# Kernel tuning notes

Measured on AMD Instinct MI355X. Metric: run time of the kernel, lower is better.

## Reference

```python
import jax, jax.numpy as jnp
import numpy as np

ROUTING_ITERS = 3
EPS = 1e-9


def squash(s, axis=-1):
    sq_norm = jnp.sum(s * s, axis=axis, keepdims=True)
    scale = sq_norm / (1.0 + sq_norm)
    return scale * s / jnp.sqrt(sq_norm + EPS)


def setup_inputs() -> dict:
    key = jax.random.key(0)
    k_u, k_w = jax.random.split(key)
    B, P, C, OUT, IN = 256, 2048, 10, 16, 8
    u = jax.random.normal(k_u, (B, P, IN), dtype=jnp.float32)
    W = 0.01 * jax.random.normal(k_w, (1, P, C, OUT, IN), dtype=jnp.float32)
    return {"u": u, "W": W}


def reference(u, W):
    # u: [B, P, IN], W: [1, P, C, OUT, IN]
    # u_hat[b,p,c,o] = sum_i W[0,p,c,o,i] * u[b,p,i]
    u_hat = jnp.einsum('pcoi,bpi->bpco', W[0], u)  # [B, P, C, OUT]
    B, P, C, _ = u_hat.shape
    b = jnp.zeros((B, P, C), dtype=u_hat.dtype)
    v = None
    for _ in range(ROUTING_ITERS):
        c = jax.nn.softmax(b, axis=2)                     # [B, P, C]
        s = jnp.einsum('bpc,bpco->bco', c, u_hat)         # [B, C, OUT]
        v = squash(s, axis=-1)                            # [B, C, OUT]
        b = b + jnp.einsum('bpco,bco->bpc', u_hat, v)     # agreement update
    return v
```

## Files before the change

kernel.cpp:

```cpp
#include <hip/hip_runtime.h>
#include <hip/hip_fp16.h>


#define Bn 256
#define Pn 2048
#define Cn 10
#define On 16
#define In 8
#define ROW 160
#define BT 64
#define PPB 16
#define NPT (Pn / PPB)
#define TPB 512
#define GRID ((Bn / BT) * NPT)

typedef _Float16 f16x8 __attribute__((ext_vector_type(8)));
typedef _Float16 h2f __attribute__((ext_vector_type(2)));
typedef float f32x4 __attribute__((ext_vector_type(4)));

__device__ __forceinline__ void gl_lds16(const void* g, void* l) {
  __builtin_amdgcn_global_load_lds(
      (const __attribute__((address_space(1))) unsigned int*)g,
      (__attribute__((address_space(3))) unsigned int*)l, 16, 0, 0);
}

__device__ __forceinline__ h2f pack2(float a, float b) {
  __half2 t = __floats2half2_rn(a, b);
  return *reinterpret_cast<h2f*>(&t);
}

__global__ __launch_bounds__(256) void k_prepw(const float* __restrict__ W,
                                               _Float16* __restrict__ Wh) {
  const size_t base = (size_t)blockIdx.x * 1280;
#pragma unroll
  for (int r = 0; r < 5; ++r) {
    const int i = threadIdx.x + 256 * r;
    Wh[base + i] = (_Float16)W[base + i];
  }
}

__global__ __launch_bounds__(256) void k_prepu(const float* __restrict__ u,
                                               _Float16* __restrict__ uT) {
  const int p2 = blockIdx.x * 2;
  const int b = threadIdx.x;
  const float4* src = reinterpret_cast<const float4*>(u + ((size_t)b * Pn + p2) * In);
  const float4 q0 = src[0], q1 = src[1], q2 = src[2], q3 = src[3];
  f16x8 o0, o1;
  o0[0] = (_Float16)q0.x; o0[1] = (_Float16)q0.y; o0[2] = (_Float16)q0.z; o0[3] = (_Float16)q0.w;
  o0[4] = (_Float16)q1.x; o0[5] = (_Float16)q1.y; o0[6] = (_Float16)q1.z; o0[7] = (_Float16)q1.w;
  o1[0] = (_Float16)q2.x; o1[1] = (_Float16)q2.y; o1[2] = (_Float16)q2.z; o1[3] = (_Float16)q2.w;
  o1[4] = (_Float16)q3.x; o1[5] = (_Float16)q3.y; o1[6] = (_Float16)q3.z; o1[7] = (_Float16)q3.w;
  *reinterpret_cast<f16x8*>(uT + ((size_t)p2 * Bn + b) * In) = o0;
  *reinterpret_cast<f16x8*>(uT + ((size_t)(p2 + 1) * Bn + b) * In) = o1;
}

template <int MODE>
__global__ __launch_bounds__(TPB, 2) void k_cap(const _Float16* __restrict__ uT,
                                                const _Float16* __restrict__ Wh,
                                                const float* __restrict__ s1,
                                                const float* __restrict__ s2,
                                                float* __restrict__ part) {
  __shared__ float arena[10368];
  _Float16* wH = reinterpret_cast<_Float16*>(arena);
  const int x = blockIdx.x;
  const int bt = x >> 7;
  const int pt = x & 127;
  const int tid = threadIdx.x;
  const int w = tid >> 6;
  const int pg = w >> 2;
  const int wq = w & 3;
  const int lane = tid & 63;
  const int col = lane & 15;
  const int quad = lane >> 4;
  const int b = bt * BT + wq * 16 + col;
  const int p0 = pt * PPB;

  {
    const char* src = reinterpret_cast<const char*>(Wh + (size_t)p0 * 1280);
    char* dst = reinterpret_cast<char*>(wH);
#pragma unroll
    for (int r = 0; r < 5; ++r)
      gl_lds16(src + r * 8192 + tid * 16, dst + r * 8192 + tid * 16);
  }

  h2f vh[Cn][2];
  if (MODE >= 1) {
    const float4* spA = reinterpret_cast<const float4*>(s1 + (size_t)b * ROW);
    const float4* spB = reinterpret_cast<const float4*>(s2 + (size_t)b * ROW);
#pragma unroll
    for (int c = 0; c < Cn; ++c) {
      const float4 a0 = spA[c * 4 + 0], a1 = spA[c * 4 + 1];
      const float4 a2 = spA[c * 4 + 2], a3 = spA[c * 4 + 3];
      float sqA = a0.x * a0.x + a0.y * a0.y + a0.z * a0.z + a0.w * a0.w;
      sqA += a1.x * a1.x + a1.y * a1.y + a1.z * a1.z + a1.w * a1.w;
      sqA += a2.x * a2.x + a2.y * a2.y + a2.z * a2.z + a2.w * a2.w;
      sqA += a3.x * a3.x + a3.y * a3.y + a3.z * a3.z + a3.w * a3.w;
      sqA *= 0.01f;
      const float facA = 0.1f * (sqA / (1.f + sqA)) / sqrtf(sqA + 1e-9f);
      const float4 qa = spA[c * 4 + quad];
      float v0 = facA * qa.x, v1_ = facA * qa.y;
      float v2_ = facA * qa.z, v3_ = facA * qa.w;
      if (MODE == 2) {
        const float4 b0 = spB[c * 4 + 0], b1 = spB[c * 4 + 1];
        const float4 b2 = spB[c * 4 + 2], b3 = spB[c * 4 + 3];
        float sqB = b0.x * b0.x + b0.y * b0.y + b0.z * b0.z + b0.w * b0.w;
        sqB += b1.x * b1.x + b1.y * b1.y + b1.z * b1.z + b1.w * b1.w;
        sqB += b2.x * b2.x + b2.y * b2.y + b2.z * b2.z + b2.w * b2.w;
        sqB += b3.x * b3.x + b3.y * b3.y + b3.z * b3.z + b3.w * b3.w;
        const float facB = (sqB / (1.f + sqB)) / sqrtf(sqB + 1e-9f);
        const float4 qb = spB[c * 4 + quad];
        v0 += facB * qb.x; v1_ += facB * qb.y;
        v2_ += facB * qb.z; v3_ += facB * qb.w;
      }
      vh[c][0] = pack2(v0, v1_);
      vh[c][1] = pack2(v2_, v3_);
    }
  }

  f32x4 acc[Cn];
  const f32x4 zc = {0.f, 0.f, 0.f, 0.f};
#pragma unroll
  for (int c = 0; c < Cn; ++c) acc[c] = zc;

  const _Float16* urow = uT + ((size_t)(p0 + pg * 8) * Bn + b) * In;
  f16x8 uf = *reinterpret_cast<const f16x8*>(urow);
  const f16x8 zb = {0, 0, 0, 0, 0, 0, 0, 0};
  const bool isq0 = (quad == 0);

  __syncthreads();

  for (int ip = 0; ip < 8; ++ip) {
    f16x8 ufn = uf;
    if (ip + 1 < 8)
      ufn = *reinterpret_cast<const f16x8*>(urow + (size_t)(ip + 1) * Bn * In);
    const f16x8 ub = isq0 ? uf : zb;
    const _Float16* wp = wH + (pg * 8 + ip) * 1280 + col * 8;

    if (MODE == 0) {
#pragma unroll
      for (int c = 0; c < Cn; ++c) {
        const f16x8 aW = *reinterpret_cast<const f16x8*>(wp + c * 128);
        acc[c] = __builtin_amdgcn_mfma_f32_16x16x32_f16(aW, ub, acc[c], 0, 0, 0);
      }
    } else {
      float lf[Cn];
      h2f uhh[Cn][2];
#pragma unroll
      for (int c = 0; c < Cn; ++c) {
        const f16x8 aW = *reinterpret_cast<const f16x8*>(wp + c * 128);
        const f32x4 uh =
            __builtin_amdgcn_mfma_f32_16x16x32_f16(aW, ub, zc, 0, 0, 0);
        float lp = uh[0] * (float)vh[c][0][0];
        lp = __builtin_fmaf(uh[1], (float)vh[c][0][1], lp);
        lp = __builtin_fmaf(uh[2], (float)vh[c][1][0], lp);
        lp = __builtin_fmaf(uh[3], (float)vh[c][1][1], lp);
        lf[c] = lp;
        uhh[c][0] = pack2(uh[0], uh[1]);
        uhh[c][1] = pack2(uh[2], uh[3]);
      }
#pragma unroll
      for (int c = 0; c < Cn; ++c) {
        lf[c] += __shfl_xor(lf[c], 16, 64);
        lf[c] += __shfl_xor(lf[c], 32, 64);
      }
      float m = fmaxf(fmaxf(__builtin_fmaf(0.f, 0.f, lf[0]), lf[1]), lf[2]);
      m = fmaxf(m, fmaxf(fmaxf(lf[3], lf[4]), fmaxf(lf[5], lf[6])));
      m = fmaxf(m, fmaxf(fmaxf(lf[7], lf[8]), lf[9]));
      float ss = 0.f;
#pragma unroll
      for (int c = 0; c < Cn; ++c) {
        lf[c] = __expf(lf[c] - m);
        ss += lf[c];
      }
      const float inv = 1.f / ss;
#pragma unroll
      for (int c = 0; c < Cn; ++c) {
        const float cv = lf[c] * inv;
        acc[c][0] = __builtin_fmaf(cv, (float)uhh[c][0][0], acc[c][0]);
        acc[c][1] = __builtin_fmaf(cv, (float)uhh[c][0][1], acc[c][1]);
        acc[c][2] = __builtin_fmaf(cv, (float)uhh[c][1][0], acc[c][2]);
        acc[c][3] = __builtin_fmaf(cv, (float)uhh[c][1][1], acc[c][3]);
      }
    }
    uf = ufn;
  }

  __syncthreads();
  float* sAcc = arena;
  const int row = wq * 16 + col;
  if (pg == 1) {
    float* dst = &sAcc[row * 162 + quad * 4];
#pragma unroll
    for (int c = 0; c < Cn; ++c)
      *reinterpret_cast<f32x4*>(dst + c * 16) = acc[c];
  }
  __syncthreads();
  if (pg == 0) {
    const float* srcp = &sAcc[row * 162 + quad * 4];
    float* pb = part + ((size_t)x * BT + row) * ROW;
#pragma unroll
    for (int c = 0; c < Cn; ++c) {
      f32x4 t = *reinterpret_cast<const f32x4*>(srcp + c * 16);
      t = t + acc[c];
      *reinterpret_cast<f32x4*>(pb + c * 16 + quad * 4) = t;
    }
  }
}

__global__ __launch_bounds__(256) void k_red(const float* __restrict__ part,
                                             float* __restrict__ s) {
  const int cell = blockIdx.x * 256 + threadIdx.x;
  const int chunk = blockIdx.y;
  const int b = cell / 160, rem = cell - 160 * b;
  const int bt = b >> 6, bl = b & 63;
  const float* p0 =
      part + ((size_t)(bt * NPT + chunk * 32) * BT + bl) * ROW + rem;
  float a0 = 0.f, a1 = 0.f, a2 = 0.f, a3 = 0.f;
  float a4 = 0.f, a5 = 0.f, a6 = 0.f, a7 = 0.f;
#pragma unroll
  for (int pt = 0; pt < 32; pt += 8) {
    a0 += p0[(size_t)(pt + 0) * BT * ROW];
    a1 += p0[(size_t)(pt + 1) * BT * ROW];
    a2 += p0[(size_t)(pt + 2) * BT * ROW];
    a3 += p0[(size_t)(pt + 3) * BT * ROW];
    a4 += p0[(size_t)(pt + 4) * BT * ROW];
    a5 += p0[(size_t)(pt + 5) * BT * ROW];
    a6 += p0[(size_t)(pt + 6) * BT * ROW];
    a7 += p0[(size_t)(pt + 7) * BT * ROW];
  }
  atomicAdd(&s[cell], ((a0 + a1) + (a2 + a3)) + ((a4 + a5) + (a6 + a7)));
}

__global__ __launch_bounds__(256) void k_out(const float* __restrict__ s,
                                             float* __restrict__ out) {
  const int gi = blockIdx.x * 256 + threadIdx.x;
  const int b = gi / 10, c = gi - 10 * b;
  const float* sp = s + (size_t)b * ROW + c * 16;
  float sq = 0.f;
#pragma unroll
  for (int o = 0; o < On; ++o) { const float xx = sp[o]; sq += xx * xx; }
  const float fac = (sq / (1.f + sq)) / sqrtf(sq + 1e-9f);
  float* op = out + (size_t)b * ROW + c * 16;
#pragma unroll
  for (int o = 0; o < On; ++o) op[o] = fac * sp[o];
}

extern "C" void kernel_launch(void* const* d_in, const int* in_sizes, int n_in,
                              void* d_out, int out_size, void* d_ws, size_t ws_size,
                              hipStream_t stream) {
  (void)in_sizes; (void)n_in; (void)out_size;
  const float* u = (const float*)d_in[0];
  const float* W = (const float*)d_in[1];
  float* out = (float*)d_out;
  float* s1 = (float*)d_ws;
  float* s2 = s1 + (size_t)Bn * ROW;
  float* s3 = s2 + (size_t)Bn * ROW;
  float* part = s3 + (size_t)Bn * ROW;
  _Float16* Wh = (_Float16*)(part + (size_t)GRID * BT * ROW);
  _Float16* uTp = Wh + (size_t)Pn * Cn * On * In;
  const size_t need =
      ((size_t)3 * Bn * ROW + (size_t)GRID * BT * ROW) * sizeof(float) +
      ((size_t)Pn * Cn * On * In + (size_t)Pn * Bn * In) * sizeof(_Float16);
  if (ws_size < need) return;
  hipMemsetAsync(s1, 0, (size_t)3 * Bn * ROW * sizeof(float), stream);
  k_prepw<<<Pn, 256, 0, stream>>>(W, Wh);
  k_prepu<<<Pn / 2, 256, 0, stream>>>(u, uTp);
  k_cap<0><<<GRID, TPB, 0, stream>>>(uTp, Wh, s1, s1, part);
  k_red<<<dim3(160, 4), 256, 0, stream>>>(part, s1);
  k_cap<1><<<GRID, TPB, 0, stream>>>(uTp, Wh, s1, s1, part);
  k_red<<<dim3(160, 4), 256, 0, stream>>>(part, s2);
  k_cap<2><<<GRID, TPB, 0, stream>>>(uTp, Wh, s1, s2, part);
  k_red<<<dim3(160, 4), 256, 0, stream>>>(part, s3);
  k_out<<<10, 256, 0, stream>>>(s3, out);
}
```

Measured before the change: 224.7 us.

## Halve k_cap block size, loop all 16 P per wave, drop LDS cross-group reduction

The capsule kernel now runs 256 threads (4 waves) per block instead of 512. Each wave processes all 16 P values, two at a time, rather than splitting them between two wave groups. This removes the shared-memory reduction and its two extra barriers at the end, and gives each wave two independent MFMA/softmax chains per iteration for more instruction-level parallelism. The costs are fewer waves per block, higher register pressure from doubled live state, and a longer serial loop per wave.

```diff
diff --git a/kernel.cpp b/kernel.cpp
--- a/kernel.cpp
+++ b/kernel.cpp
@@ -11,7 +11,7 @@
 #define BT 64
 #define PPB 16
 #define NPT (Pn / PPB)
-#define TPB 512
+#define TPB 256
 #define GRID ((Bn / BT) * NPT)
 
 typedef _Float16 f16x8 __attribute__((ext_vector_type(8)));
@@ -60,27 +60,24 @@
                                                 const float* __restrict__ s1,
                                                 const float* __restrict__ s2,
                                                 float* __restrict__ part) {
-  __shared__ float arena[10368];
-  _Float16* wH = reinterpret_cast<_Float16*>(arena);
+  __shared__ _Float16 wH[PPB * 1280];
   const int x = blockIdx.x;
   const int bt = x >> 7;
   const int pt = x & 127;
   const int tid = threadIdx.x;
   const int w = tid >> 6;
-  const int pg = w >> 2;
-  const int wq = w & 3;
   const int lane = tid & 63;
   const int col = lane & 15;
   const int quad = lane >> 4;
-  const int b = bt * BT + wq * 16 + col;
+  const int b = bt * BT + w * 16 + col;
   const int p0 = pt * PPB;
 
   {
     const char* src = reinterpret_cast<const char*>(Wh + (size_t)p0 * 1280);
     char* dst = reinterpret_cast<char*>(wH);
 #pragma unroll
-    for (int r = 0; r < 5; ++r)
-      gl_lds16(src + r * 8192 + tid * 16, dst + r * 8192 + tid * 16);
+    for (int r = 0; r < 10; ++r)
+      gl_lds16(src + r * 4096 + tid * 16, dst + r * 4096 + tid * 16);
   }
 
   h2f vh[Cn][2];
@@ -122,89 +119,104 @@
 #pragma unroll
   for (int c = 0; c < Cn; ++c) acc[c] = zc;
 
-  const _Float16* urow = uT + ((size_t)(p0 + pg * 8) * Bn + b) * In;
-  f16x8 uf = *reinterpret_cast<const f16x8*>(urow);
+  const _Float16* urow = uT + ((size_t)p0 * Bn + b) * In;
+  f16x8 ufA = *reinterpret_cast<const f16x8*>(urow);
+  f16x8 ufB = *reinterpret_cast<const f16x8*>(urow + (size_t)Bn * In);
   const f16x8 zb = {0, 0, 0, 0, 0, 0, 0, 0};
   const bool isq0 = (quad == 0);
 
   __syncthreads();
 
-  for (int ip = 0; ip < 8; ++ip) {
-    f16x8 ufn = uf;
-    if (ip + 1 < 8)
-      ufn = *reinterpret_cast<const f16x8*>(urow + (size_t)(ip + 1) * Bn * In);
-    const f16x8 ub = isq0 ? uf : zb;
-    const _Float16* wp = wH + (pg * 8 + ip) * 1280 + col * 8;
+  for (int ip = 0; ip < PPB; ip += 2) {
+    f16x8 nfA = ufA, nfB = ufB;
+    if (ip + 2 < PPB) {
+      nfA = *reinterpret_cast<const f16x8*>(urow + (size_t)(ip + 2) * Bn * In);
+      nfB = *reinterpret_cast<const f16x8*>(urow + (size_t)(ip + 3) * Bn * In);
+    }
+    const f16x8 ubA = isq0 ? ufA : zb;
+    const f16x8 ubB = isq0 ? ufB : zb;
+    const _Float16* wpA = wH + (size_t)ip * 1280 + col * 8;
+    const _Float16* wpB = wpA + 1280;
 
     if (MODE == 0) {
 #pragma unroll
       for (int c = 0; c < Cn; ++c) {
-        const f16x8 aW = *reinterpret_cast<const f16x8*>(wp + c * 128);
-        acc[c] = __builtin_amdgcn_mfma_f32_16x16x32_f16(aW, ub, acc[c], 0, 0, 0);
+        const f16x8 aWA = *reinterpret_cast<const f16x8*>(wpA + c * 128);
+        const f16x8 aWB = *reinterpret_cast<const f16x8*>(wpB + c * 128);
+        acc[c] = __builtin_amdgcn_mfma_f32_16x16x32_f16(aWA, ubA, acc[c], 0, 0, 0);
+        acc[c] = __builtin_amdgcn_mfma_f32_16x16x32_f16(aWB, ubB, acc[c], 0, 0, 0);
       }
     } else {
-      float lf[Cn];
-      h2f uhh[Cn][2];
-#pragma unroll
-      for (int c = 0; c < Cn; ++c) {
-        const f16x8 aW = *reinterpret_cast<const f16x8*>(wp + c * 128);
-        const f32x4 uh =
-            __builtin_amdgcn_mfma_f32_16x16x32_f16(aW, ub, zc, 0, 0, 0);
-        float lp = uh[0] * (float)vh[c][0][0];
-        lp = __builtin_fmaf(uh[1], (float)vh[c][0][1], lp);
-        lp = __builtin_fmaf(uh[2], (float)vh[c][1][0], lp);
-        lp = __builtin_fmaf(uh[3], (float)vh[c][1][1], lp);
-        lf[c] = lp;
-        uhh[c][0] = pack2(uh[0], uh[1]);
-        uhh[c][1] = pack2(uh[2], uh[3]);
-      }
-#pragma unroll
-      for (int c = 0; c < Cn; ++c) {
-        lf[c] += __shfl_xor(lf[c], 16, 64);
-        lf[c] += __shfl_xor(lf[c], 32, 64);
-      }
-      float m = fmaxf(fmaxf(__builtin_fmaf(0.f, 0.f, lf[0]), lf[1]), lf[2]);
-      m = fmaxf(m, fmaxf(fmaxf(lf[3], lf[4]), fmaxf(lf[5], lf[6])));
-      m = fmaxf(m, fmaxf(fmaxf(lf[7], lf[8]), lf[9]));
-      float ss = 0.f;
-#pragma unroll
-      for (int c = 0; c < Cn; ++c) {
-        lf[c] = __expf(lf[c] - m);
-        ss += lf[c];
-      }
-      const float inv = 1.f / ss;
-#pragma unroll
-      for (int c = 0; c < Cn; ++c) {
-        const float cv = lf[c] * inv;
-        acc[c][0] = __builtin_fmaf(cv, (float)uhh[c][0][0], acc[c][0]);
-        acc[c][1] = __builtin_fmaf(cv, (float)uhh[c][0][1], acc[c][1]);
-        acc[c][2] = __builtin_fmaf(cv, (float)uhh[c][1][0], acc[c][2]);
-        acc[c][3] = __builtin_fmaf(cv, (float)uhh[c][1][1], acc[c][3]);
+      float lfA[Cn], lfB[Cn];
+      h2f uhA[Cn][2], uhB[Cn][2];
+#pragma unroll
+      for (int c = 0; c < Cn; ++c) {
+        const f16x8 aWA = *reinterpret_cast<const f16x8*>(wpA + c * 128);
+        const f16x8 aWB = *reinterpret_cast<const f16x8*>(wpB + c * 128);
+        const f32x4 dA =
+            __builtin_amdgcn_mfma_f32_16x16x32_f16(aWA, ubA, zc, 0, 0, 0);
+        const f32x4 dB =
+            __builtin_amdgcn_mfma_f32_16x16x32_f16(aWB, ubB, zc, 0, 0, 0);
+        float la = dA[0] * (float)vh[c][0][0];
+        la = __builtin_fmaf(dA[1], (float)vh[c][0][1], la);
+        la = __builtin_fmaf(dA[2], (float)vh[c][1][0], la);
+        la = __builtin_fmaf(dA[3], (float)vh[c][1][1], la);
+        lfA[c] = la;
+        float lb = dB[0] * (float)vh[c][0][0];
+        lb = __builtin_fmaf(dB[1], (float)vh[c][0][1], lb);
+        lb = __builtin_fmaf(dB[2], (float)vh[c][1][0], lb);
+        lb = __builtin_fmaf(dB[3], (float)vh[c][1][1], lb);
+        lfB[c] = lb;
+        uhA[c][0] = pack2(dA[0], dA[1]);
+        uhA[c][1] = pack2(dA[2], dA[3]);
+        uhB[c][0] = pack2(dB[0], dB[1]);
+        uhB[c][1] = pack2(dB[2], dB[3]);
+      }
+#pragma unroll
+      for (int c = 0; c < Cn; ++c) {
+        lfA[c] += __shfl_xor(lfA[c], 16, 64);
+        lfB[c] += __shfl_xor(lfB[c], 16, 64);
+        lfA[c] += __shfl_xor(lfA[c], 32, 64);
+        lfB[c] += __shfl_xor(lfB[c], 32, 64);
+      }
+      float mA = fmaxf(fmaxf(lfA[0], lfA[1]), fmaxf(lfA[2], lfA[3]));
+      float mB = fmaxf(fmaxf(lfB[0], lfB[1]), fmaxf(lfB[2], lfB[3]));
+      mA = fmaxf(mA, fmaxf(fmaxf(lfA[4], lfA[5]), fmaxf(lfA[6], lfA[7])));
+      mB = fmaxf(mB, fmaxf(fmaxf(lfB[4], lfB[5]), fmaxf(lfB[6], lfB[7])));
+      mA = fmaxf(mA, fmaxf(lfA[8], lfA[9]));
+      mB = fmaxf(mB, fmaxf(lfB[8], lfB[9]));
+      float ssA = 0.f, ssB = 0.f;
+#pragma unroll
+      for (int c = 0; c < Cn; ++c) {
+        lfA[c] = __expf(lfA[c] - mA);
+        ssA += lfA[c];
+        lfB[c] = __expf(lfB[c] - mB);
+        ssB += lfB[c];
+      }
+      const float invA = 1.f / ssA;
+      const float invB = 1.f / ssB;
+#pragma unroll
+      for (int c = 0; c < Cn; ++c) {
+        const float cvA = lfA[c] * invA;
+        const float cvB = lfB[c] * invB;
+        float t0 = __builtin_fmaf(cvA, (float)uhA[c][0][0], acc[c][0]);
+        float t1 = __builtin_fmaf(cvA, (float)uhA[c][0][1], acc[c][1]);
+        float t2 = __builtin_fmaf(cvA, (float)uhA[c][1][0], acc[c][2]);
+        float t3 = __builtin_fmaf(cvA, (float)uhA[c][1][1], acc[c][3]);
+        acc[c][0] = __builtin_fmaf(cvB, (float)uhB[c][0][0], t0);
+        acc[c][1] = __builtin_fmaf(cvB, (float)uhB[c][0][1], t1);
+        acc[c][2] = __builtin_fmaf(cvB, (float)uhB[c][1][0], t2);
+        acc[c][3] = __builtin_fmaf(cvB, (float)uhB[c][1][1], t3);
       }
     }
-    uf = ufn;
-  }
-
-  __syncthreads();
-  float* sAcc = arena;
-  const int row = wq * 16 + col;
-  if (pg == 1) {
-    float* dst = &sAcc[row * 162 + quad * 4];
-#pragma unroll
-    for (int c = 0; c < Cn; ++c)
-      *reinterpret_cast<f32x4*>(dst + c * 16) = acc[c];
-  }
-  __syncthreads();
-  if (pg == 0) {
-    const float* srcp = &sAcc[row * 162 + quad * 4];
-    float* pb = part + ((size_t)x * BT + row) * ROW;
-#pragma unroll
-    for (int c = 0; c < Cn; ++c) {
-      f32x4 t = *reinterpret_cast<const f32x4*>(srcp + c * 16);
-      t = t + acc[c];
-      *reinterpret_cast<f32x4*>(pb + c * 16 + quad * 4) = t;
-    }
-  }
+    ufA = nfA;
+    ufB = nfB;
+  }
+
+  float* pb = part + ((size_t)x * BT + w * 16 + col) * ROW;
+#pragma unroll
+  for (int c = 0; c < Cn; ++c)
+    *reinterpret_cast<f32x4*>(pb + c * 16 + quad * 4) = acc[c];
 }
 
 __global__ __launch_bounds__(256) void k_red(const float* __restrict__ part,
```

Result: faster. 184.4 us (-17.9%).

## Restructure capsule routing to independent per-wave tiles with precomputed squashed v

Applied to the files above, without the earlier changes.

Drops the LDS staging of W and the cross-wave LDS reduction in the routing kernel. Each wave now handles its own 16-batch by 8-capsule tile, reads W straight from global memory, and writes its partial sums straight out, which doubles the partial buffer and the reduction chunks. A new small kernel computes the squashed v vectors once in fp16, so the main kernel no longer recomputes the squash norms in every block. The cost is more global and L2 traffic for W, because it is no longer shared across waves through LDS, and a larger reduction over partials.

```diff
diff --git a/kernel.cpp b/kernel.cpp
--- a/kernel.cpp
+++ b/kernel.cpp
@@ -8,21 +8,14 @@
 #define On 16
 #define In 8
 #define ROW 160
-#define BT 64
-#define PPB 16
-#define NPT (Pn / PPB)
-#define TPB 512
-#define GRID ((Bn / BT) * NPT)
+#define PPW 8
+#define NPT (Pn / PPW)
+#define TPB 256
+#define GRID (16 * NPT / 4)
 
 typedef _Float16 f16x8 __attribute__((ext_vector_type(8)));
 typedef _Float16 h2f __attribute__((ext_vector_type(2)));
 typedef float f32x4 __attribute__((ext_vector_type(4)));
-
-__device__ __forceinline__ void gl_lds16(const void* g, void* l) {
-  __builtin_amdgcn_global_load_lds(
-      (const __attribute__((address_space(1))) unsigned int*)g,
-      (__attribute__((address_space(3))) unsigned int*)l, 16, 0, 0);
-}
 
 __device__ __forceinline__ h2f pack2(float a, float b) {
   __half2 t = __floats2half2_rn(a, b);
@@ -54,66 +47,74 @@
   *reinterpret_cast<f16x8*>(uT + ((size_t)(p2 + 1) * Bn + b) * In) = o1;
 }
 
+template <int M>
+__global__ __launch_bounds__(256) void k_vprep(const float* __restrict__ sA,
+                                               const float* __restrict__ sB,
+                                               _Float16* __restrict__ vT) {
+  const int g = blockIdx.x * 256 + threadIdx.x;
+  const int b = g / 10, c = g - 10 * b;
+  const float4* pa = reinterpret_cast<const float4*>(sA + (size_t)b * ROW + c * 16);
+  const float4 a0 = pa[0], a1 = pa[1], a2 = pa[2], a3 = pa[3];
+  float sqA = a0.x * a0.x + a0.y * a0.y + a0.z * a0.z + a0.w * a0.w;
+  sqA += a1.x * a1.x + a1.y * a1.y + a1.z * a1.z + a1.w * a1.w;
+  sqA += a2.x * a2.x + a2.y * a2.y + a2.z * a2.z + a2.w * a2.w;
+  sqA += a3.x * a3.x + a3.y * a3.y + a3.z * a3.z + a3.w * a3.w;
+  sqA *= 0.01f;
+  const float facA = 0.1f * (sqA / (1.f + sqA)) / sqrtf(sqA + 1e-9f);
+  float v[16] = {facA * a0.x, facA * a0.y, facA * a0.z, facA * a0.w,
+                 facA * a1.x, facA * a1.y, facA * a1.z, facA * a1.w,
+                 facA * a2.x, facA * a2.y, facA * a2.z, facA * a2.w,
+                 facA * a3.x, facA * a3.y, facA * a3.z, facA * a3.w};
+  if (M == 2) {
+    const float4* pb = reinterpret_cast<const float4*>(sB + (size_t)b * ROW + c * 16);
+    const float4 b0 = pb[0], b1 = pb[1], b2 = pb[2], b3 = pb[3];
+    float sqB = b0.x * b0.x + b0.y * b0.y + b0.z * b0.z + b0.w * b0.w;
+    sqB += b1.x * b1.x + b1.y * b1.y + b1.z * b1.z + b1.w * b1.w;
+    sqB += b2.x * b2.x + b2.y * b2.y + b2.z * b2.z + b2.w * b2.w;
+    sqB += b3.x * b3.x + b3.y * b3.y + b3.z * b3.z + b3.w * b3.w;
+    const float facB = (sqB / (1.f + sqB)) / sqrtf(sqB + 1e-9f);
+    v[0] += facB * b0.x; v[1] += facB * b0.y; v[2] += facB * b0.z; v[3] += facB * b0.w;
+    v[4] += facB * b1.x; v[5] += facB * b1.y; v[6] += facB * b1.z; v[7] += facB * b1.w;
+    v[8] += facB * b2.x; v[9] += facB * b2.y; v[10] += facB * b2.z; v[11] += facB * b2.w;
+    v[12] += facB * b3.x; v[13] += facB * b3.y; v[14] += facB * b3.z; v[15] += facB * b3.w;
+  }
+#pragma unroll
+  for (int q = 0; q < 4; ++q) {
+    union { h2f h[2]; uint2 u2; } o;
+    o.h[0] = pack2(v[q * 4 + 0], v[q * 4 + 1]);
+    o.h[1] = pack2(v[q * 4 + 2], v[q * 4 + 3]);
+    *reinterpret_cast<uint2*>(vT + (size_t)((b * 4 + q) * 10 + c) * 4) = o.u2;
+  }
+}
+
 template <int MODE>
-__global__ __launch_bounds__(TPB, 2) void k_cap(const _Float16* __restrict__ uT,
-                                                const _Float16* __restrict__ Wh,
-                                                const float* __restrict__ s1,
-                                                const float* __restrict__ s2,
-                                                float* __restrict__ part) {
-  __shared__ float arena[10368];
-  _Float16* wH = reinterpret_cast<_Float16*>(arena);
+__global__ __launch_bounds__(TPB) void k_cap(const _Float16* __restrict__ uT,
+                                             const _Float16* __restrict__ Wh,
+                                             const _Float16* __restrict__ vT,
+                                             float* __restrict__ part) {
   const int x = blockIdx.x;
-  const int bt = x >> 7;
-  const int pt = x & 127;
   const int tid = threadIdx.x;
   const int w = tid >> 6;
-  const int pg = w >> 2;
-  const int wq = w & 3;
   const int lane = tid & 63;
+  const int gw = x * 4 + w;
+  const int btile = gw >> 8;
+  const int ptile = gw & 255;
   const int col = lane & 15;
   const int quad = lane >> 4;
-  const int b = bt * BT + wq * 16 + col;
-  const int p0 = pt * PPB;
-
-  {
-    const char* src = reinterpret_cast<const char*>(Wh + (size_t)p0 * 1280);
-    char* dst = reinterpret_cast<char*>(wH);
-#pragma unroll
-    for (int r = 0; r < 5; ++r)
-      gl_lds16(src + r * 8192 + tid * 16, dst + r * 8192 + tid * 16);
-  }
+  const int b = btile * 16 + col;
+  const int p0 = ptile * PPW;
 
   h2f vh[Cn][2];
   if (MODE >= 1) {
-    const float4* spA = reinterpret_cast<const float4*>(s1 + (size_t)b * ROW);
-    const float4* spB = reinterpret_cast<const float4*>(s2 + (size_t)b * ROW);
+    const f16x8* vsrc =
+        reinterpret_cast<const f16x8*>(vT + (size_t)(b * 4 + quad) * 40);
+    union { f16x8 v8[5]; h2f h[20]; } vu;
+#pragma unroll
+    for (int r = 0; r < 5; ++r) vu.v8[r] = vsrc[r];
 #pragma unroll
     for (int c = 0; c < Cn; ++c) {
-      const float4 a0 = spA[c * 4 + 0], a1 = spA[c * 4 + 1];
-      const float4 a2 = spA[c * 4 + 2], a3 = spA[c * 4 + 3];
-      float sqA = a0.x * a0.x + a0.y * a0.y + a0.z * a0.z + a0.w * a0.w;
-      sqA += a1.x * a1.x + a1.y * a1.y + a1.z * a1.z + a1.w * a1.w;
-      sqA += a2.x * a2.x + a2.y * a2.y + a2.z * a2.z + a2.w * a2.w;
-      sqA += a3.x * a3.x + a3.y * a3.y + a3.z * a3.z + a3.w * a3.w;
-      sqA *= 0.01f;
-      const float facA = 0.1f * (sqA / (1.f + sqA)) / sqrtf(sqA + 1e-9f);
-      const float4 qa = spA[c * 4 + quad];
-      float v0 = facA * qa.x, v1_ = facA * qa.y;
-      float v2_ = facA * qa.z, v3_ = facA * qa.w;
-      if (MODE == 2) {
-        const float4 b0 = spB[c * 4 + 0], b1 = spB[c * 4 + 1];
-        const float4 b2 = spB[c * 4 + 2], b3 = spB[c * 4 + 3];
-        float sqB = b0.x * b0.x + b0.y * b0.y + b0.z * b0.z + b0.w * b0.w;
-        sqB += b1.x * b1.x + b1.y * b1.y + b1.z * b1.z + b1.w * b1.w;
-        sqB += b2.x * b2.x + b2.y * b2.y + b2.z * b2.z + b2.w * b2.w;
-        sqB += b3.x * b3.x + b3.y * b3.y + b3.z * b3.z + b3.w * b3.w;
-        const float facB = (sqB / (1.f + sqB)) / sqrtf(sqB + 1e-9f);
-        const float4 qb = spB[c * 4 + quad];
-        v0 += facB * qb.x; v1_ += facB * qb.y;
-        v2_ += facB * qb.z; v3_ += facB * qb.w;
-      }
-      vh[c][0] = pack2(v0, v1_);
-      vh[c][1] = pack2(v2_, v3_);
+      vh[c][0] = vu.h[2 * c];
+      vh[c][1] = vu.h[2 * c + 1];
     }
   }
 
@@ -122,19 +123,16 @@
 #pragma unroll
   for (int c = 0; c < Cn; ++c) acc[c] = zc;
 
-  const _Float16* urow = uT + ((size_t)(p0 + pg * 8) * Bn + b) * In;
-  f16x8 uf = *reinterpret_cast<const f16x8*>(urow);
   const f16x8 zb = {0, 0, 0, 0, 0, 0, 0, 0};
   const bool isq0 = (quad == 0);
 
-  __syncthreads();
-
-  for (int ip = 0; ip < 8; ++ip) {
-    f16x8 ufn = uf;
-    if (ip + 1 < 8)
-      ufn = *reinterpret_cast<const f16x8*>(urow + (size_t)(ip + 1) * Bn * In);
+#pragma unroll 2
+  for (int ip = 0; ip < PPW; ++ip) {
+    const int p = p0 + ip;
+    const _Float16* wp = Wh + (size_t)p * 1280 + col * 8;
+    const f16x8 uf =
+        *reinterpret_cast<const f16x8*>(uT + ((size_t)p * Bn + b) * In);
     const f16x8 ub = isq0 ? uf : zb;
-    const _Float16* wp = wH + (pg * 8 + ip) * 1280 + col * 8;
 
     if (MODE == 0) {
 #pragma unroll
@@ -148,24 +146,24 @@
 #pragma unroll
       for (int c = 0; c < Cn; ++c) {
         const f16x8 aW = *reinterpret_cast<const f16x8*>(wp + c * 128);
-        const f32x4 uh =
+        const f32x4 d =
             __builtin_amdgcn_mfma_f32_16x16x32_f16(aW, ub, zc, 0, 0, 0);
-        float lp = uh[0] * (float)vh[c][0][0];
-        lp = __builtin_fmaf(uh[1], (float)vh[c][0][1], lp);
-        lp = __builtin_fmaf(uh[2], (float)vh[c][1][0], lp);
-        lp = __builtin_fmaf(uh[3], (float)vh[c][1][1], lp);
+        float lp = d[0] * (float)vh[c][0][0];
+        lp = __builtin_fmaf(d[1], (float)vh[c][0][1], lp);
+        lp = __builtin_fmaf(d[2], (float)vh[c][1][0], lp);
+        lp = __builtin_fmaf(d[3], (float)vh[c][1][1], lp);
         lf[c] = lp;
-        uhh[c][0] = pack2(uh[0], uh[1]);
-        uhh[c][1] = pack2(uh[2], uh[3]);
+        uhh[c][0] = pack2(d[0], d[1]);
+        uhh[c][1] = pack2(d[2], d[3]);
       }
 #pragma unroll
       for (int c = 0; c < Cn; ++c) {
         lf[c] += __shfl_xor(lf[c], 16, 64);
         lf[c] += __shfl_xor(lf[c], 32, 64);
       }
-      float m = fmaxf(fmaxf(__builtin_fmaf(0.f, 0.f, lf[0]), lf[1]), lf[2]);
-      m = fmaxf(m, fmaxf(fmaxf(lf[3], lf[4]), fmaxf(lf[5], lf[6])));
-      m = fmaxf(m, fmaxf(fmaxf(lf[7], lf[8]), lf[9]));
+      float m = fmaxf(fmaxf(lf[0], lf[1]), fmaxf(lf[2], lf[3]));
+      m = fmaxf(m, fmaxf(fmaxf(lf[4], lf[5]), fmaxf(lf[6], lf[7])));
+      m = fmaxf(m, fmaxf(lf[8], lf[9]));
       float ss = 0.f;
 #pragma unroll
       for (int c = 0; c < Cn; ++c) {
@@ -182,29 +180,12 @@
         acc[c][3] = __builtin_fmaf(cv, (float)uhh[c][1][1], acc[c][3]);
       }
     }
-    uf = ufn;
-  }
-
-  __syncthreads();
-  float* sAcc = arena;
-  const int row = wq * 16 + col;
-  if (pg == 1) {
-    float* dst = &sAcc[row * 162 + quad * 4];
-#pragma unroll
-    for (int c = 0; c < Cn; ++c)
-      *reinterpret_cast<f32x4*>(dst + c * 16) = acc[c];
-  }
-  __syncthreads();
-  if (pg == 0) {
-    const float* srcp = &sAcc[row * 162 + quad * 4];
-    float* pb = part + ((size_t)x * BT + row) * ROW;
-#pragma unroll
-    for (int c = 0; c < Cn; ++c) {
-      f32x4 t = *reinterpret_cast<const f32x4*>(srcp + c * 16);
-      t = t + acc[c];
-      *reinterpret_cast<f32x4*>(pb + c * 16 + quad * 4) = t;
-    }
-  }
+  }
+
+  float* pb = part + ((size_t)ptile * Bn + b) * ROW;
+#pragma unroll
+  for (int c = 0; c < Cn; ++c)
+    *reinterpret_cast<f32x4*>(pb + c * 16 + quad * 4) = acc[c];
 }
 
 __global__ __launch_bounds__(256) void k_red(const float* __restrict__ part,
@@ -212,21 +193,21 @@
   const int cell = blockIdx.x * 256 + threadIdx.x;
   const int chunk = blockIdx.y;
   const int b = cell / 160, rem = cell - 160 * b;
-  const int bt = b >> 6, bl = b & 63;
   const float* p0 =
-      part + ((size_t)(bt * NPT + chunk * 32) * BT + bl) * ROW + rem;
+      part + ((size_t)(chunk * 32) * Bn + b) * ROW + rem;
+  const size_t step = (size_t)Bn * ROW;
   float a0 = 0.f, a1 = 0.f, a2 = 0.f, a3 = 0.f;
   float a4 = 0.f, a5 = 0.f, a6 = 0.f, a7 = 0.f;
 #pragma unroll
   for (int pt = 0; pt < 32; pt += 8) {
-    a0 += p0[(size_t)(pt + 0) * BT * ROW];
-    a1 += p0[(size_t)(pt + 1) * BT * ROW];
-    a2 += p0[(size_t)(pt + 2) * BT * ROW];
-    a3 += p0[(size_t)(pt + 3) * BT * ROW];
-    a4 += p0[(size_t)(pt + 4) * BT * ROW];
-    a5 += p0[(size_t)(pt + 5) * BT * ROW];
-    a6 += p0[(size_t)(pt + 6) * BT * ROW];
-    a7 += p0[(size_t)(pt + 7) * BT * ROW];
+    a0 += p0[(pt + 0) * step];
+    a1 += p0[(pt + 1) * step];
+    a2 += p0[(pt + 2) * step];
+    a3 += p0[(pt + 3) * step];
+    a4 += p0[(pt + 4) * step];
+    a5 += p0[(pt + 5) * step];
+    a6 += p0[(pt + 6) * step];
+    a7 += p0[(pt + 7) * step];
   }
   atomicAdd(&s[cell], ((a0 + a1) + (a2 + a3)) + ((a4 + a5) + (a6 + a7)));
 }
@@ -256,20 +237,24 @@
   float* s2 = s1 + (size_t)Bn * ROW;
   float* s3 = s2 + (size_t)Bn * ROW;
   float* part = s3 + (size_t)Bn * ROW;
-  _Float16* Wh = (_Float16*)(part + (size_t)GRID * BT * ROW);
+  _Float16* Wh = (_Float16*)(part + (size_t)NPT * Bn * ROW);
   _Float16* uTp = Wh + (size_t)Pn * Cn * On * In;
+  _Float16* vT = uTp + (size_t)Pn * Bn * In;
   const size_t need =
-      ((size_t)3 * Bn * ROW + (size_t)GRID * BT * ROW) * sizeof(float) +
-      ((size_t)Pn * Cn * On * In + (size_t)Pn * Bn * In) * sizeof(_Float16);
+      ((size_t)3 * Bn * ROW + (size_t)NPT * Bn * ROW) * sizeof(float) +
+      ((size_t)Pn * Cn * On * In + (size_t)Pn * Bn * In + (size_t)Bn * 4 * 40) *
+          sizeof(_Float16);
   if (ws_size < need) return;
   hipMemsetAsync(s1, 0, (size_t)3 * Bn * ROW * sizeof(float), stream);
   k_prepw<<<Pn, 256, 0, stream>>>(W, Wh);
   k_prepu<<<Pn / 2, 256, 0, stream>>>(u, uTp);
-  k_cap<0><<<GRID, TPB, 0, stream>>>(uTp, Wh, s1, s1, part);
-  k_red<<<dim3(160, 4), 256, 0, stream>>>(part, s1);
-  k_cap<1><<<GRID, TPB, 0, stream>>>(uTp, Wh, s1, s1, part);
-  k_red<<<dim3(160, 4), 256, 0, stream>>>(part, s2);
-  k_cap<2><<<GRID, TPB, 0, stream>>>(uTp, Wh, s1, s2, part);
-  k_red<<<dim3(160, 4), 256, 0, stream>>>(part, s3);
+  k_cap<0><<<GRID, TPB, 0, stream>>>(uTp, Wh, vT, part);
+  k_red<<<dim3(160, 8), 256, 0, stream>>>(part, s1);
+  k_vprep<1><<<10, 256, 0, stream>>>(s1, s1, vT);
+  k_cap<1><<<GRID, TPB, 0, stream>>>(uTp, Wh, vT, part);
+  k_red<<<dim3(160, 8), 256, 0, stream>>>(part, s2);
+  k_vprep<2><<<10, 256, 0, stream>>>(s1, s2, vT);
+  k_cap<2><<<GRID, TPB, 0, stream>>>(uTp, Wh, vT, part);
+  k_red<<<dim3(160, 8), 256, 0, stream>>>(part, s3);
   k_out<<<10, 256, 0, stream>>>(s3, out);
 }
```

New measurement: 233.1 us. +3.7%, slower.
